# Performance work log

Hardware: AMD Instinct MI355X
Metric: run time of the kernel (lower is better)

The kernel has to match this reference:

```python
import jax, jax.numpy as jnp
import numpy as np

H = 16        # num attention heads
KVH = 4       # num key/value heads
D = 128       # head dim
WIN = 1024    # sliding window (in packed per-state positions)
THETA = 10000.0
NUM_STATES = 8


def rotate_half(x):
    half = x.shape[-1] // 2
    return jnp.concatenate([-x[..., half:], x[..., :half]], axis=-1)


def setup_inputs() -> dict:
    key = jax.random.key(0)
    ks = jax.random.split(key, 6)
    B, L, HID = 2, 2048, 2048
    s = 0.02
    hidden_states = jax.random.normal(ks[0], (B, L, HID), jnp.float32)
    Wq = jax.random.normal(ks[1], (H * D, HID), jnp.float32) * s
    Wk = jax.random.normal(ks[2], (KVH * D, HID), jnp.float32) * s
    Wv = jax.random.normal(ks[3], (KVH * D, HID), jnp.float32) * s
    Wo = jax.random.normal(ks[4], (HID, H * D), jnp.float32) * s
    sid = jax.random.randint(ks[5], (B, L), 0, NUM_STATES).astype(jnp.int64)
    position_ids = jnp.tile(jnp.arange(L, dtype=jnp.int64)[None, :], (B, 1))
    return dict(hidden_states=hidden_states, Wq=Wq, Wk=Wk, Wv=Wv, Wo=Wo,
                sid=sid, position_ids=position_ids)


def reference(hidden_states, Wq, Wk, Wv, Wo, sid, position_ids):
    B, L, HID = hidden_states.shape
    # projections (Linear without bias: x @ W.T)
    q = (hidden_states @ Wq.T).reshape(B, L, H, D)
    k = (hidden_states @ Wk.T).reshape(B, L, KVH, D)
    v = (hidden_states @ Wv.T).reshape(B, L, KVH, D)
    # rotary embedding
    inv_freq = 1.0 / (THETA ** (jnp.arange(0, D, 2, dtype=jnp.float32) / D))
    freqs = position_ids.astype(jnp.float32)[:, :, None] * inv_freq[None, None, :]  # [B,L,D/2]
    emb = jnp.concatenate([freqs, freqs], axis=-1)                                  # [B,L,D]
    cos = jnp.cos(emb)[:, :, None, :].astype(hidden_states.dtype)
    sin = jnp.sin(emb)[:, :, None, :].astype(hidden_states.dtype)
    q = q * cos + rotate_half(q) * sin
    k = k * cos + rotate_half(k) * sin
    # GQA: repeat kv heads (repeat_interleave along head dim)
    n_rep = H // KVH
    k = jnp.repeat(k, n_rep, axis=2)  # [B,L,H,D]
    v = jnp.repeat(v, n_rep, axis=2)
    # BoSs mask: attend within same state id, causal, sliding window over
    # packed-per-state rank distance (equivalent to the varlen packing path)
    same = sid[:, :, None] == sid[:, None, :]                  # [B,L,L]
    tril = jnp.tril(jnp.ones((L, L), dtype=bool))[None]        # [1,L,L]
    rank = jnp.sum(same & tril, axis=-1) - 1                   # [B,L] rank within own state
    win_ok = (rank[:, :, None] - rank[:, None, :]) <= WIN
    mask = same & tril & win_ok                                # [B,L,L]
    scale = D ** -0.5
    scores = jnp.einsum('bqhd,bkhd->bhqk', q, k) * scale       # [B,H,L,L]
    scores = jnp.where(mask[:, None, :, :], scores, jnp.finfo(scores.dtype).min)
    attn = jax.nn.softmax(scores, axis=-1)
    o = jnp.einsum('bhqk,bkhd->bqhd', attn, v).reshape(B, L, H * D)
    return o @ Wo.T
```

## Files before the change

### kernel.cpp

```cpp
#include <hip/hip_runtime.h>
#include <hip/hip_bf16.h>

#define H_ 16
#define KVH_ 4
#define D_ 128
#define L_ 2048
#define B_ 2
#define HID_ 2048
#define WIN_ 1024
#define NS_ 8
#define QKV_N 3072

typedef __attribute__((ext_vector_type(8))) short short8;
typedef __attribute__((ext_vector_type(4))) float floatx4;

__device__ inline float bf16_to_f(unsigned short u) {
    union { unsigned int i; float f; } c; c.i = ((unsigned int)u) << 16; return c.f;
}
__device__ inline unsigned short f_to_bf16(float f) {
    __hip_bfloat16 h = __float2bfloat16(f);
    return *(unsigned short*)&h;
}

__device__ inline int world_is_bf16(const unsigned short* hs_u) {
    int lane = threadIdx.x & 63;
    unsigned short u = hs_u[(lane & 31) * 2];
    int e = (u >> 7) & 0xFF;
    unsigned long long bad = __ballot(e > 130);
    return bad == 0ULL;
}
__device__ inline int pid_stride(const int* pids) { return (pids[1] == 0) ? 2 : 1; }

__global__ __launch_bounds__(256) void convert_all(const void* __restrict__ hs,
                                                   const void* __restrict__ Wq,
                                                   const void* __restrict__ Wk,
                                                   const void* __restrict__ Wv,
                                                   const void* __restrict__ Wo,
                                                   unsigned short* __restrict__ c_hs,
                                                   unsigned short* __restrict__ c_Wq,
                                                   unsigned short* __restrict__ c_Wk,
                                                   unsigned short* __restrict__ c_Wv,
                                                   unsigned short* __restrict__ c_Wo) {
    int isbf = world_is_bf16((const unsigned short*)hs);
    const int N0 = (B_ * L_ * HID_) / 4;
    const int N1 = (HID_ * HID_) / 4;
    const int N2 = (KVH_ * D_ * HID_) / 4;
    const int N3 = N2;
    const int N4 = N1;
    const int total = N0 + N1 + N2 + N3 + N4;
    for (int i = blockIdx.x * 256 + threadIdx.x; i < total; i += gridDim.x * 256) {
        int j = i;
        const void* src; unsigned short* dst;
        if (j < N0)              { src = hs; dst = c_hs; }
        else if ((j -= N0) < N1) { src = Wq; dst = c_Wq; }
        else if ((j -= N1) < N2) { src = Wk; dst = c_Wk; }
        else if ((j -= N2) < N3) { src = Wv; dst = c_Wv; }
        else                     { j -= N3; src = Wo; dst = c_Wo; }
        if (isbf) {
            ((ushort4*)dst)[j] = ((const ushort4*)src)[j];
        } else {
            float4 f = ((const float4*)src)[j];
            ushort4 o4;
            o4.x = f_to_bf16(f.x); o4.y = f_to_bf16(f.y);
            o4.z = f_to_bf16(f.z); o4.w = f_to_bf16(f.w);
            ((ushort4*)dst)[j] = o4;
        }
    }
}

__global__ __launch_bounds__(256) void scan_kernel(const int* __restrict__ sid,
                                                   const int* __restrict__ pids,
                                                   int* __restrict__ rank,
                                                   int* __restrict__ poslist,
                                                   int* __restrict__ counts) {
    int stride = pid_stride(pids);
    int b = blockIdx.x;
    int t = threadIdx.x;
    __shared__ int cnt[256][NS_];
    __shared__ int pre[256][NS_];
    const int* s = sid + (size_t)b * L_ * stride;
    int myid[8];
#pragma unroll
    for (int i = 0; i < 8; i++) myid[i] = s[(t * 8 + i) * stride];
#pragma unroll
    for (int st = 0; st < NS_; st++) cnt[t][st] = 0;
#pragma unroll
    for (int i = 0; i < 8; i++) cnt[t][myid[i]]++;
    __syncthreads();
    for (int off = 1; off < 256; off <<= 1) {
        int add[NS_];
        if (t >= off)
#pragma unroll
            for (int st = 0; st < NS_; st++) add[st] = cnt[t - off][st];
        __syncthreads();
        if (t >= off)
#pragma unroll
            for (int st = 0; st < NS_; st++) cnt[t][st] += add[st];
        __syncthreads();
    }
#pragma unroll
    for (int st = 0; st < NS_; st++) pre[t][st] = t ? cnt[t - 1][st] : 0;
    if (t == 255)
#pragma unroll
        for (int st = 0; st < NS_; st++) counts[b * NS_ + st] = cnt[255][st];
    __syncthreads();
#pragma unroll
    for (int i = 0; i < 8; i++) {
        int sd = myid[i];
        int r = pre[t][sd]++;
        int pos = t * 8 + i;
        rank[b * L_ + pos] = r;
        poslist[((size_t)b * NS_ + sd) * L_ + r] = pos;
    }
}

#define STAGE(gptr, ldsdst)                                                     \
    __builtin_amdgcn_global_load_lds(                                           \
        (const __attribute__((address_space(1))) unsigned int*)(gptr),          \
        (__attribute__((address_space(3))) unsigned int*)(ldsdst), 16, 0, 0)

#define SB __builtin_amdgcn_sched_barrier(0)

#define MFMA_P(P)                                                               \
    __builtin_amdgcn_s_setprio(1);                                              \
    _Pragma("unroll")                                                           \
    for (int m2 = 0; m2 < 2; ++m2)                                              \
        _Pragma("unroll")                                                       \
        for (int nt = 0; nt < 4; ++nt)                                          \
            acc[(P) * 2 + m2][nt] = __builtin_amdgcn_mfma_f32_16x16x32_bf16(    \
                fA[(P) * 2 + m2], fB[nt], acc[(P) * 2 + m2][nt], 0, 0, 0);      \
    __builtin_amdgcn_s_setprio(0)

template<int MT>
__global__ __launch_bounds__(512, 1) void gemm_t(const unsigned short* __restrict__ A,
                                                 const unsigned short* __restrict__ B0,
                                                 const unsigned short* __restrict__ B1,
                                                 const unsigned short* __restrict__ B2,
                                                 void* __restrict__ C,
                                                 int M, int N, int K,
                                                 int nb1, int nb2,
                                                 const unsigned short* __restrict__ hs_probe,
                                                 int c_mode) {
    const int CH_A = MT / 2;
    __shared__ unsigned short As[4][MT * 2048];
    __shared__ unsigned short Bs[4][8192];
    int tid = threadIdx.x;
    int wave = tid >> 6, lane = tid & 63;
    int quad = lane >> 4, l16 = lane & 15;
    int wr = wave >> 2, wc = wave & 3;
    int bn_t = blockIdx.x;
    int bm = blockIdx.y * (MT * 64), bn = bn_t * 256;

    const unsigned short* Bseg;
    int brow0;
    if (bn_t < nb1)      { Bseg = B0; brow0 = bn; }
    else if (bn_t < nb2) { Bseg = B1; brow0 = bn - nb1 * 256; }
    else                 { Bseg = B2; brow0 = bn - nb2 * 256; }

    int sub = tid >> 2, slot = tid & 3;
    int swz = slot ^ ((sub >> 1) & 3);
    unsigned int a_off[CH_A], b_off[2];
#pragma unroll
    for (int c = 0; c < CH_A; ++c)
        a_off[c] = (unsigned int)((bm + c * 128 + sub) * K + swz * 8);
#pragma unroll
    for (int c = 0; c < 2; ++c)
        b_off[c] = (unsigned int)((brow0 + c * 128 + sub) * K + swz * 8);

    const int arow = wr * (MT * 32) + l16;
    const int brr  = wc * 64 + l16;
    const int xr   = (l16 >> 1) & 3;

    floatx4 acc[2 * MT][4] = {};
    short8 fA[2 * MT], fB[4];
    const int KT = K >> 5;

#pragma unroll
    for (int pt = 0; pt < 3; ++pt) {
        unsigned int kel = (unsigned int)pt * 32;
#pragma unroll
        for (int c = 0; c < 2; ++c)
            STAGE(Bseg + b_off[c] + kel, &Bs[pt][c * 4096 + tid * 8]);
#pragma unroll
        for (int c = 0; c < CH_A; ++c)
            STAGE(A + a_off[c] + kel, &As[pt][c * 4096 + tid * 8]);
    }

    for (int t = 0; t < KT; ++t) {
        const unsigned short* Ab = As[t & 3];
        const unsigned short* Bb = Bs[t & 3];
        int nbuf = (t + 3) & 3;
        int t3 = (t + 3 < KT) ? t + 3 : KT - 1;
        unsigned int kel = (unsigned int)t3 * 32;

        if constexpr (MT == 4) asm volatile("s_waitcnt vmcnt(8)" ::: "memory");
        else                   asm volatile("s_waitcnt vmcnt(6)" ::: "memory");
        __builtin_amdgcn_s_barrier();
        asm volatile("" ::: "memory");

#pragma unroll
        for (int nt = 0; nt < 4; ++nt)
            fB[nt] = *(const short8*)&Bb[(brr + nt * 16) * 32 + ((quad ^ xr) * 8)];
#pragma unroll
        for (int mt = 0; mt < 2 * MT; ++mt)
            fA[mt] = *(const short8*)&Ab[(arow + mt * 16) * 32 + ((quad ^ xr) * 8)];
        SB;

#pragma unroll
        for (int c = 0; c < 2; ++c)
            STAGE(Bseg + b_off[c] + kel, &Bs[nbuf][c * 4096 + tid * 8]);
#pragma unroll
        for (int c = 0; c < CH_A; ++c)
            STAGE(A + a_off[c] + kel, &As[nbuf][c * 4096 + tid * 8]);
        SB;

        MFMA_P(0); SB;
        MFMA_P(1);
        if constexpr (MT == 4) {
            SB; MFMA_P(2); SB; MFMA_P(3);
        }
    }
    asm volatile("s_waitcnt vmcnt(0)" ::: "memory");

    int cf32 = c_mode ? !world_is_bf16(hs_probe) : 0;
#pragma unroll
    for (int a = 0; a < 2 * MT; ++a)
#pragma unroll
        for (int g = 0; g < 4; ++g)
#pragma unroll
            for (int r = 0; r < 4; ++r) {
                int row = bm + wr * (MT * 32) + a * 16 + quad * 4 + r;
                int col = bn + wc * 64 + g * 16 + l16;
                size_t idx = (size_t)row * N + col;
                if (cf32) ((float*)C)[idx] = acc[a][g][r];
                else      ((unsigned short*)C)[idx] = f_to_bf16(acc[a][g][r]);
            }
}

__global__ __launch_bounds__(256) void rope_kernel(unsigned short* __restrict__ qkv,
                                                   const int* __restrict__ pos_ids) {
    int stride = pid_stride(pos_ids);
    int idx = blockIdx.x * 256 + threadIdx.x;
    int i = idx & 63;
    int tmp = idx >> 6;
    int head = tmp % 20;
    int bl = tmp / 20;
    if (bl >= B_ * L_) return;
    float posf = (float)pos_ids[bl * stride];
    float inv = exp2f(-(float)i * (2.0f / 128.0f) * 13.287712379549449f);
    float ang = posf * inv;
    float c = cosf(ang), sn = sinf(ang);
    unsigned short* p = qkv + (size_t)bl * QKV_N +
                        ((head < H_) ? head * D_ : 2048 + (head - H_) * D_);
    float x0 = bf16_to_f(p[i]), x1 = bf16_to_f(p[i + 64]);
    p[i]      = f_to_bf16(x0 * c - x1 * sn);
    p[i + 64] = f_to_bf16(x1 * c + x0 * sn);
}

__global__ __launch_bounds__(256, 4) void attn_mfma(const unsigned short* __restrict__ qkv,
                                                    const int* __restrict__ counts,
                                                    const int* __restrict__ poslist,
                                                    unsigned short* __restrict__ o) {
    int qt  = blockIdx.x & 127;
    int kvh = (blockIdx.x >> 7) & 3;
    int s   = (blockIdx.x >> 9) & 7;
    int b   = blockIdx.x >> 12;
    int n = counts[b * NS_ + s];
    if (qt * 16 >= n) return;
    const int* plist = poslist + ((size_t)b * NS_ + s) * L_;

    __shared__ short Ksh[32][136];
    __shared__ short Vsh[128][40];
    __shared__ short Psh[4][16][40];
    __shared__ int posq[16];

    int tid = threadIdx.x;
    int wave = tid >> 6, lane = tid & 63;
    int quad = lane >> 4, l16 = lane & 15;
    int h = kvh * 4 + wave;
    const float scale = 0.08838834764831845f;

    if (tid < 16) posq[tid] = plist[min(qt * 16 + tid, n - 1)];
    __syncthreads();

    short8 qf[4];
    {
        const unsigned short* gq =
            qkv + ((size_t)(b << 11) + posq[l16]) * QKV_N + h * D_;
#pragma unroll
        for (int kk = 0; kk < 4; kk++)
            qf[kk] = *(const short8*)(gq + kk * 32 + quad * 8);
    }

    float m_r[4], l_r[4];
    floatx4 Ov[8];
#pragma unroll
    for (int r4 = 0; r4 < 4; r4++) { m_r[r4] = -1e30f; l_r[r4] = 0.f; }
#pragma unroll
    for (int nt = 0; nt < 8; nt++) Ov[nt] = (floatx4){0.f, 0.f, 0.f, 0.f};

    int c0 = max(0, (qt * 16 - WIN_) >> 5);
    int nch = ((qt * 16 + 15) >> 5) + 1;

    int r = tid >> 3, seg = tid & 7;
    int vc = r ^ ((seg & 3) << 3);
    short8 kr0, kr1, vr0, vr1;
    {
        int kpos = plist[min(c0 * 32 + r, n - 1)];
        size_t base = ((size_t)(b << 11) + kpos) * QKV_N + 2048 + kvh * D_ + seg * 16;
        kr0 = *(const short8*)(qkv + base);
        kr1 = *(const short8*)(qkv + base + 8);
        vr0 = *(const short8*)(qkv + base + 512);
        vr1 = *(const short8*)(qkv + base + 520);
    }

    for (int c = c0; c < nch; c++) {
        *(short8*)&Ksh[r][seg * 16]     = kr0;
        *(short8*)&Ksh[r][seg * 16 + 8] = kr1;
#pragma unroll
        for (int e = 0; e < 8; e++) Vsh[seg * 16 + e][vc] = vr0[e];
#pragma unroll
        for (int e = 0; e < 8; e++) Vsh[seg * 16 + 8 + e][vc] = vr1[e];
        __syncthreads();

        if (c + 1 < nch) {
            int kpos = plist[min((c + 1) * 32 + r, n - 1)];
            size_t base = ((size_t)(b << 11) + kpos) * QKV_N + 2048 + kvh * D_ + seg * 16;
            kr0 = *(const short8*)(qkv + base);
            kr1 = *(const short8*)(qkv + base + 8);
            vr0 = *(const short8*)(qkv + base + 512);
            vr1 = *(const short8*)(qkv + base + 520);
        }

        floatx4 s0 = (floatx4){0.f, 0.f, 0.f, 0.f};
        floatx4 s1 = (floatx4){0.f, 0.f, 0.f, 0.f};
#pragma unroll
        for (int kk = 0; kk < 4; kk++) {
            short8 kfa = *(const short8*)&Ksh[l16][kk * 32 + quad * 8];
            s0 = __builtin_amdgcn_mfma_f32_16x16x32_bf16(qf[kk], kfa, s0, 0, 0, 0);
        }
#pragma unroll
        for (int kk = 0; kk < 4; kk++) {
            short8 kfb = *(const short8*)&Ksh[16 + l16][kk * 32 + quad * 8];
            s1 = __builtin_amdgcn_mfma_f32_16x16x32_bf16(qf[kk], kfb, s1, 0, 0, 0);
        }

        int kr0i = c * 32 + l16, kr1i = kr0i + 16;
        float x0[4], x1[4], rmax[4];
#pragma unroll
        for (int r4 = 0; r4 < 4; r4++) {
            int qr = qt * 16 + quad * 4 + r4;
            bool mk0 = (kr0i <= qr) && (kr0i >= qr - WIN_);
            bool mk1 = (kr1i <= qr) && (kr1i >= qr - WIN_);
            x0[r4] = mk0 ? s0[r4] * scale : -1e30f;
            x1[r4] = mk1 ? s1[r4] * scale : -1e30f;
            rmax[r4] = fmaxf(x0[r4], x1[r4]);
        }
#pragma unroll
        for (int st = 1; st <= 8; st <<= 1)
#pragma unroll
            for (int r4 = 0; r4 < 4; r4++)
                rmax[r4] = fmaxf(rmax[r4], __shfl_xor(rmax[r4], st, 64));
        float al[4], psum[4];
#pragma unroll
        for (int r4 = 0; r4 < 4; r4++) {
            float nm = fmaxf(m_r[r4], rmax[r4]);
            al[r4] = __expf(m_r[r4] - nm);
            m_r[r4] = nm;
            x0[r4] = (x0[r4] > -1e29f) ? __expf(x0[r4] - nm) : 0.f;
            x1[r4] = (x1[r4] > -1e29f) ? __expf(x1[r4] - nm) : 0.f;
            psum[r4] = x0[r4] + x1[r4];
        }
#pragma unroll
        for (int st = 1; st <= 8; st <<= 1)
#pragma unroll
            for (int r4 = 0; r4 < 4; r4++)
                psum[r4] += __shfl_xor(psum[r4], st, 64);
#pragma unroll
        for (int r4 = 0; r4 < 4; r4++) l_r[r4] = l_r[r4] * al[r4] + psum[r4];
#pragma unroll
        for (int nt = 0; nt < 8; nt++)
#pragma unroll
            for (int r4 = 0; r4 < 4; r4++) Ov[nt][r4] *= al[r4];

#pragma unroll
        for (int r4 = 0; r4 < 4; r4++) {
            Psh[wave][quad * 4 + r4][l16]      = (short)f_to_bf16(x0[r4]);
            Psh[wave][quad * 4 + r4][16 + l16] = (short)f_to_bf16(x1[r4]);
        }
        short8 pf = *(const short8*)&Psh[wave][l16][quad * 8];

#pragma unroll
        for (int nt = 0; nt < 8; nt++) {
            short8 vf = *(const short8*)&Vsh[nt * 16 + l16][(quad ^ (nt & 3)) * 8];
            Ov[nt] = __builtin_amdgcn_mfma_f32_16x16x32_bf16(pf, vf, Ov[nt], 0, 0, 0);
        }
        __syncthreads();
    }

    float inv_r[4];
    int pos_r[4], qvalid[4];
#pragma unroll
    for (int r4 = 0; r4 < 4; r4++) {
        int qr = qt * 16 + quad * 4 + r4;
        qvalid[r4] = (qr < n);
        inv_r[r4] = 1.f / l_r[r4];
        pos_r[r4] = posq[quad * 4 + r4];
    }
#pragma unroll
    for (int nt = 0; nt < 8; nt++)
#pragma unroll
        for (int r4 = 0; r4 < 4; r4++)
            if (qvalid[r4])
                o[(((size_t)(b << 11) + pos_r[r4]) * H_ + h) * D_ + nt * 16 + l16] =
                    f_to_bf16(Ov[nt][r4] * inv_r[r4]);
}

extern "C" void kernel_launch(void* const* d_in, const int* in_sizes, int n_in,
                              void* d_out, int out_size, void* d_ws, size_t ws_size,
                              hipStream_t stream) {
    const void* hs = d_in[0];
    const void* Wq = d_in[1];
    const void* Wk = d_in[2];
    const void* Wv = d_in[3];
    const void* Wo = d_in[4];
    const int* sid  = (const int*)d_in[5];
    const int* pids = (const int*)d_in[6];

    const int M = B_ * L_;
    char* w = (char*)d_ws;
    unsigned short* qkv  = (unsigned short*)(w + 256);
    unsigned short* o_b  = (unsigned short*)(w + 25166080);
    unsigned short* c_hs = (unsigned short*)(w + 41943296);
    unsigned short* c_Wq = (unsigned short*)(w + 58720512);
    unsigned short* c_Wk = (unsigned short*)(w + 67109120);
    unsigned short* c_Wv = (unsigned short*)(w + 69206272);
    unsigned short* c_Wo = (unsigned short*)(w + 71303424);
    int* rank            = (int*)(w + 79692032);
    int* plist           = (int*)(w + 79708416);
    int* counts          = (int*)(w + 79839488);

    const unsigned short* hs_probe = (const unsigned short*)hs;

    convert_all<<<2048, 256, 0, stream>>>(hs, Wq, Wk, Wv, Wo,
                                          c_hs, c_Wq, c_Wk, c_Wv, c_Wo);

    scan_kernel<<<B_, 256, 0, stream>>>(sid, pids, rank, plist, counts);

    gemm_t<4><<<dim3(QKV_N / 256, M / 256), 512, 0, stream>>>(
        c_hs, c_Wq, c_Wk, c_Wv, qkv, M, QKV_N, HID_, 8, 10, hs_probe, 0);

    int rope_threads = M * (H_ + KVH_) * 64;
    rope_kernel<<<(rope_threads + 255) / 256, 256, 0, stream>>>(qkv, pids);

    attn_mfma<<<B_ * NS_ * KVH_ * (L_ / 16), 256, 0, stream>>>(qkv, counts, plist, o_b);

    gemm_t<2><<<dim3(HID_ / 256, M / 128), 512, 0, stream>>>(
        o_b, c_Wo, c_Wo, c_Wo, d_out, M, HID_, HID_, 1 << 30, 1 << 30, hs_probe, 1);
}
```

Measured before the change: 295.1 us.

## Skip bf16 copy pass and split GEMM A-fragment loads around MFMA halves

```diff
diff --git a/kernel.cpp b/kernel.cpp
--- a/kernel.cpp
+++ b/kernel.cpp
@@ -42,6 +42,7 @@
                                                    unsigned short* __restrict__ c_Wv,
                                                    unsigned short* __restrict__ c_Wo) {
     int isbf = world_is_bf16((const unsigned short*)hs);
+    if (isbf) return;
     const int N0 = (B_ * L_ * HID_) / 4;
     const int N1 = (HID_ * HID_) / 4;
     const int N2 = (KVH_ * D_ * HID_) / 4;
@@ -56,15 +57,11 @@
         else if ((j -= N1) < N2) { src = Wk; dst = c_Wk; }
         else if ((j -= N2) < N3) { src = Wv; dst = c_Wv; }
         else                     { j -= N3; src = Wo; dst = c_Wo; }
-        if (isbf) {
-            ((ushort4*)dst)[j] = ((const ushort4*)src)[j];
-        } else {
-            float4 f = ((const float4*)src)[j];
-            ushort4 o4;
-            o4.x = f_to_bf16(f.x); o4.y = f_to_bf16(f.y);
-            o4.z = f_to_bf16(f.z); o4.w = f_to_bf16(f.w);
-            ((ushort4*)dst)[j] = o4;
-        }
+        float4 f = ((const float4*)src)[j];
+        ushort4 o4;
+        o4.x = f_to_bf16(f.x); o4.y = f_to_bf16(f.y);
+        o4.z = f_to_bf16(f.z); o4.w = f_to_bf16(f.w);
+        ((ushort4*)dst)[j] = o4;
     }
 }
 
@@ -120,22 +117,17 @@
         (__attribute__((address_space(3))) unsigned int*)(ldsdst), 16, 0, 0)
 
 #define SB __builtin_amdgcn_sched_barrier(0)
-
-#define MFMA_P(P)                                                               \
-    __builtin_amdgcn_s_setprio(1);                                              \
-    _Pragma("unroll")                                                           \
-    for (int m2 = 0; m2 < 2; ++m2)                                              \
-        _Pragma("unroll")                                                       \
-        for (int nt = 0; nt < 4; ++nt)                                          \
-            acc[(P) * 2 + m2][nt] = __builtin_amdgcn_mfma_f32_16x16x32_bf16(    \
-                fA[(P) * 2 + m2], fB[nt], acc[(P) * 2 + m2][nt], 0, 0, 0);      \
-    __builtin_amdgcn_s_setprio(0)
+#define LGKM0() do { asm volatile("s_waitcnt lgkmcnt(0)" ::: "memory"); SB; } while (0)
 
 template<int MT>
-__global__ __launch_bounds__(512, 1) void gemm_t(const unsigned short* __restrict__ A,
-                                                 const unsigned short* __restrict__ B0,
-                                                 const unsigned short* __restrict__ B1,
-                                                 const unsigned short* __restrict__ B2,
+__global__ __launch_bounds__(512, 1) void gemm_t(const unsigned short* __restrict__ Ac,
+                                                 const unsigned short* __restrict__ B0c,
+                                                 const unsigned short* __restrict__ B1c,
+                                                 const unsigned short* __restrict__ B2c,
+                                                 const unsigned short* __restrict__ Aa,
+                                                 const unsigned short* __restrict__ B0a,
+                                                 const unsigned short* __restrict__ B1a,
+                                                 const unsigned short* __restrict__ B2a,
                                                  void* __restrict__ C,
                                                  int M, int N, int K,
                                                  int nb1, int nb2,
@@ -151,6 +143,12 @@
     int bn_t = blockIdx.x;
     int bm = blockIdx.y * (MT * 64), bn = bn_t * 256;
 
+    int isbf = world_is_bf16(hs_probe);
+    const unsigned short* A  = isbf ? Aa  : Ac;
+    const unsigned short* B0 = isbf ? B0a : B0c;
+    const unsigned short* B1 = isbf ? B1a : B1c;
+    const unsigned short* B2 = isbf ? B2a : B2c;
+
     const unsigned short* Bseg;
     int brow0;
     if (bn_t < nb1)      { Bseg = B0; brow0 = bn; }
@@ -172,7 +170,7 @@
     const int xr   = (l16 >> 1) & 3;
 
     floatx4 acc[2 * MT][4] = {};
-    short8 fA[2 * MT], fB[4];
+    short8 fA[MT], fA2[MT], fB[4];
     const int KT = K >> 5;
 
 #pragma unroll
@@ -202,27 +200,43 @@
         for (int nt = 0; nt < 4; ++nt)
             fB[nt] = *(const short8*)&Bb[(brr + nt * 16) * 32 + ((quad ^ xr) * 8)];
 #pragma unroll
-        for (int mt = 0; mt < 2 * MT; ++mt)
+        for (int mt = 0; mt < MT; ++mt)
             fA[mt] = *(const short8*)&Ab[(arow + mt * 16) * 32 + ((quad ^ xr) * 8)];
-        SB;
-
 #pragma unroll
         for (int c = 0; c < 2; ++c)
             STAGE(Bseg + b_off[c] + kel, &Bs[nbuf][c * 4096 + tid * 8]);
+        LGKM0();
+        __builtin_amdgcn_s_setprio(1);
+#pragma unroll
+        for (int mt = 0; mt < MT; ++mt)
+#pragma unroll
+            for (int nt = 0; nt < 4; ++nt)
+                acc[mt][nt] = __builtin_amdgcn_mfma_f32_16x16x32_bf16(
+                    fA[mt], fB[nt], acc[mt][nt], 0, 0, 0);
+        __builtin_amdgcn_s_setprio(0);
+
+#pragma unroll
+        for (int mt = 0; mt < MT; ++mt)
+            fA2[mt] = *(const short8*)&Ab[(arow + (MT + mt) * 16) * 32
+                                          + ((quad ^ xr) * 8)];
 #pragma unroll
         for (int c = 0; c < CH_A; ++c)
             STAGE(A + a_off[c] + kel, &As[nbuf][c * 4096 + tid * 8]);
-        SB;
-
-        MFMA_P(0); SB;
-        MFMA_P(1);
-        if constexpr (MT == 4) {
-            SB; MFMA_P(2); SB; MFMA_P(3);
-        }
+        __builtin_amdgcn_s_barrier();
+        asm volatile("" ::: "memory");
+        LGKM0();
+        __builtin_amdgcn_s_setprio(1);
+#pragma unroll
+        for (int mt = 0; mt < MT; ++mt)
+#pragma unroll
+            for (int nt = 0; nt < 4; ++nt)
+                acc[MT + mt][nt] = __builtin_amdgcn_mfma_f32_16x16x32_bf16(
+                    fA2[mt], fB[nt], acc[MT + mt][nt], 0, 0, 0);
+        __builtin_amdgcn_s_setprio(0);
     }
     asm volatile("s_waitcnt vmcnt(0)" ::: "memory");
 
-    int cf32 = c_mode ? !world_is_bf16(hs_probe) : 0;
+    int cf32 = c_mode ? !isbf : 0;
 #pragma unroll
     for (int a = 0; a < 2 * MT; ++a)
 #pragma unroll
@@ -448,7 +462,10 @@
     scan_kernel<<<B_, 256, 0, stream>>>(sid, pids, rank, plist, counts);
 
     gemm_t<4><<<dim3(QKV_N / 256, M / 256), 512, 0, stream>>>(
-        c_hs, c_Wq, c_Wk, c_Wv, qkv, M, QKV_N, HID_, 8, 10, hs_probe, 0);
+        c_hs, c_Wq, c_Wk, c_Wv,
+        (const unsigned short*)hs, (const unsigned short*)Wq,
+        (const unsigned short*)Wk, (const unsigned short*)Wv,
+        qkv, M, QKV_N, HID_, 8, 10, hs_probe, 0);
 
     int rope_threads = M * (H_ + KVH_) * 64;
     rope_kernel<<<(rope_threads + 255) / 256, 256, 0, stream>>>(qkv, pids);
@@ -456,5 +473,8 @@
     attn_mfma<<<B_ * NS_ * KVH_ * (L_ / 16), 256, 0, stream>>>(qkv, counts, plist, o_b);
 
     gemm_t<2><<<dim3(HID_ / 256, M / 128), 512, 0, stream>>>(
-        o_b, c_Wo, c_Wo, c_Wo, d_out, M, HID_, HID_, 1 << 30, 1 << 30, hs_probe, 1);
-}
+        o_b, c_Wo, c_Wo, c_Wo,
+        o_b, (const unsigned short*)Wo, (const unsigned short*)Wo,
+        (const unsigned short*)Wo,
+        d_out, M, HID_, HID_, 1 << 30, 1 << 30, hs_probe, 1);
+}
```

New measurement: 303.9 us. +3.0%, slower.
